# Performance work log

Hardware: AMD Instinct MI355X
Metric: run time of the kernel (lower is better)

Reference implementation:

```python
import jax, jax.numpy as jnp
import numpy as np

B, H, S, D = 8, 8, 2048, 64

def setup_inputs() -> dict:
    key = jax.random.key(0)
    kq, kk, kv = jax.random.split(key, 3)
    queries = jax.random.normal(kq, (B, H, S, D), dtype=jnp.float32)
    keys = jax.random.normal(kk, (B, H, S, D), dtype=jnp.float32)
    values = jax.random.normal(kv, (B, H, S, D), dtype=jnp.float32)
    return {"queries": queries, "keys": keys, "values": values}

def reference(queries, keys, values):
    # scores: [B,H,S,S] = Q K^T / sqrt(D)
    scale = 1.0 / jnp.sqrt(jnp.asarray(queries.shape[-1], dtype=jnp.float32))
    scores = jnp.einsum('bhqd,bhkd->bhqk', queries, keys) * scale
    attn = jax.nn.softmax(scores, axis=-1)
    # dropout is identity at eval (p=0.0)
    return jnp.einsum('bhqk,bhkd->bhqd', attn, values)
```

## Files before the change

kernel.cpp:

```cpp
#include <hip/hip_runtime.h>

#define S_LEN 2048
#define HEAD_D 64
#define NH 64
#define KVB 64
#define NKT (S_LEN / KVB)
#define RS 72
#define KREG (KVB * RS)
#define IMG_USH (2 * KREG)
#define IMG_B (IMG_USH * 2)
#define WS_V5 ((size_t)NH * NKT * IMG_B)
#define IMG4_USH (KVB * HEAD_D * 2)

typedef float f32x4  __attribute__((ext_vector_type(4)));
typedef float f32x16 __attribute__((ext_vector_type(16)));
typedef __bf16 bf16x8 __attribute__((ext_vector_type(8)));

static __device__ __forceinline__ unsigned short f2bf(float x) {
  __bf16 h = (__bf16)x;
  return __builtin_bit_cast(unsigned short, h);
}
static __device__ __forceinline__ void gload_lds16(const void* g, void* l) {
  __builtin_amdgcn_global_load_lds(
      (const __attribute__((address_space(1))) unsigned int*)g,
      (__attribute__((address_space(3))) unsigned int*)l, 16, 0, 0);
}
static __device__ __forceinline__ int vpos(int kv) {
  return (kv & ~15) | (((kv >> 2) & 1) << 3) | (((kv >> 3) & 1) << 2) | (kv & 3);
}

__global__ __launch_bounds__(256) void pack_kv5(
    const float* __restrict__ K, const float* __restrict__ V,
    unsigned short* __restrict__ ws)
{
  const int kt = blockIdx.x;
  const int bh = blockIdx.y;
  const int t  = threadIdx.x;
  const float* Kg = K + ((size_t)bh * S_LEN + (size_t)kt * KVB) * HEAD_D;
  const float* Vg = V + ((size_t)bh * S_LEN + (size_t)kt * KVB) * HEAD_D;
  unsigned short* img = ws + ((size_t)bh * NKT + kt) * IMG_USH;

  __shared__ unsigned short vt[KREG];

#pragma unroll
  for (int i = 0; i < 4; ++i) {
    const int e   = t * 4 + i * 1024;
    const int row = e >> 6;
    const int col = e & 63;
    float4 k4 = *(const float4*)(Kg + e);
    ushort4 kb;
    kb.x = f2bf(k4.x); kb.y = f2bf(k4.y); kb.z = f2bf(k4.z); kb.w = f2bf(k4.w);
    *(ushort4*)&img[row * RS + col] = kb;
    float4 v4 = *(const float4*)(Vg + e);
    const int p = vpos(row);
    vt[(col + 0) * RS + p] = f2bf(v4.x);
    vt[(col + 1) * RS + p] = f2bf(v4.y);
    vt[(col + 2) * RS + p] = f2bf(v4.z);
    vt[(col + 3) * RS + p] = f2bf(v4.w);
  }
  __syncthreads();
  char* dst = (char*)(img + KREG);
  const char* src = (const char*)vt;
#pragma unroll
  for (int i = 0; i < 3; ++i) {
    const int off = t * 16 + i * 4096;
    if (off < 9216) *(uint4*)(dst + off) = *(const uint4*)(src + off);
  }
}

#define QBLK 256
__global__ __launch_bounds__(256, 2) void flash_attn_fwd_v7(
    const float* __restrict__ Q, const unsigned short* __restrict__ ws,
    float* __restrict__ O)
{
  __shared__ unsigned short lds[4][IMG_USH];

  const int tid  = threadIdx.x;
  const int wave = tid >> 6;
  const int lane = tid & 63;
  const int l31  = lane & 31;
  const int hi   = lane >> 5;

  const int bid = blockIdx.x;
  const int swz = (bid & 7) * 64 + (bid >> 3);
  const int bh  = swz >> 3;
  const int qt  = swz & 7;

  const float* Qh = Q + (size_t)bh * (S_LEN * HEAD_D);
  float*       Oh = O + (size_t)bh * (S_LEN * HEAD_D);
  const char*  gbase = (const char*)(ws + (size_t)bh * NKT * IMG_USH);

  const int qrowA = qt * QBLK + wave * 64 + l31;
  const int qrowB = qrowA + 32;

  const float K2 = 0.18033688f;
  bf16x8 qfA[4], qfB[4];
#pragma unroll
  for (int c = 0; c < 4; ++c) {
    const float* qa = Qh + (size_t)qrowA * HEAD_D + c * 16 + hi * 8;
    float4 a0 = *(const float4*)qa;
    float4 a1 = *(const float4*)(qa + 4);
    qfA[c][0] = (__bf16)(a0.x * K2); qfA[c][1] = (__bf16)(a0.y * K2);
    qfA[c][2] = (__bf16)(a0.z * K2); qfA[c][3] = (__bf16)(a0.w * K2);
    qfA[c][4] = (__bf16)(a1.x * K2); qfA[c][5] = (__bf16)(a1.y * K2);
    qfA[c][6] = (__bf16)(a1.z * K2); qfA[c][7] = (__bf16)(a1.w * K2);
    const float* qb = Qh + (size_t)qrowB * HEAD_D + c * 16 + hi * 8;
    float4 b0 = *(const float4*)qb;
    float4 b1 = *(const float4*)(qb + 4);
    qfB[c][0] = (__bf16)(b0.x * K2); qfB[c][1] = (__bf16)(b0.y * K2);
    qfB[c][2] = (__bf16)(b0.z * K2); qfB[c][3] = (__bf16)(b0.w * K2);
    qfB[c][4] = (__bf16)(b1.x * K2); qfB[c][5] = (__bf16)(b1.y * K2);
    qfB[c][6] = (__bf16)(b1.z * K2); qfB[c][7] = (__bf16)(b1.w * K2);
  }

  bf16x8 onef;
#pragma unroll
  for (int i = 0; i < 8; ++i) onef[i] = (__bf16)1.0f;

  f32x16 oaA0, oaA1, oaB0, oaB1, oaLA, oaLB;
#pragma unroll
  for (int i = 0; i < 16; ++i) {
    oaA0[i] = 0.0f; oaA1[i] = 0.0f; oaB0[i] = 0.0f; oaB1[i] = 0.0f;
    oaLA[i] = 0.0f; oaLB[i] = 0.0f;
  }

  auto stage = [&](const char* g, unsigned short* Lp) {
    char* lb = (char*)Lp;
#pragma unroll
    for (int i = 0; i < 5; ++i) {
      const int ch = wave + i * 4;
      if (ch < 18) gload_lds16(g + ch * 1024 + lane * 16, lb + ch * 1024);
    }
  };

  auto compute = [&](const unsigned short* Lp) {
    const char* ka = (const char*)Lp + l31 * 144 + hi * 16;
    f32x16 p0A, p1A, p0B, p1B;
#pragma unroll
    for (int i = 0; i < 16; ++i) { p0A[i] = 0.0f; p1A[i] = 0.0f; p0B[i] = 0.0f; p1B[i] = 0.0f; }
    __builtin_amdgcn_s_setprio(1);
#pragma unroll
    for (int c = 0; c < 4; ++c) {
      bf16x8 kf0 = *(const bf16x8*)(ka + c * 32);
      bf16x8 kf1 = *(const bf16x8*)(ka + 4608 + c * 32);
      p0A = __builtin_amdgcn_mfma_f32_32x32x16_bf16(kf0, qfA[c], p0A, 0, 0, 0);
      p0B = __builtin_amdgcn_mfma_f32_32x32x16_bf16(kf0, qfB[c], p0B, 0, 0, 0);
      p1A = __builtin_amdgcn_mfma_f32_32x32x16_bf16(kf1, qfA[c], p1A, 0, 0, 0);
      p1B = __builtin_amdgcn_mfma_f32_32x32x16_bf16(kf1, qfB[c], p1B, 0, 0, 0);
    }
    __builtin_amdgcn_s_setprio(0);

#pragma unroll
    for (int i = 0; i < 16; ++i) {
      p0A[i] = __builtin_amdgcn_exp2f(p0A[i]);
      p1A[i] = __builtin_amdgcn_exp2f(p1A[i]);
      p0B[i] = __builtin_amdgcn_exp2f(p0B[i]);
      p1B[i] = __builtin_amdgcn_exp2f(p1B[i]);
    }

    __builtin_amdgcn_s_setprio(1);
#pragma unroll
    for (int kc = 0; kc < 4; ++kc) {
      const f32x16& psA = (kc < 2) ? p0A : p1A;
      const f32x16& psB = (kc < 2) ? p0B : p1B;
      const int rb = (kc & 1) * 8;
      unsigned a0, a1, a2, a3, b0, b1, b2, b3;
      asm("v_cvt_pk_bf16_f32 %0, %1, %2" : "=v"(a0) : "v"(psA[rb + 0]), "v"(psA[rb + 1]));
      asm("v_cvt_pk_bf16_f32 %0, %1, %2" : "=v"(a1) : "v"(psA[rb + 2]), "v"(psA[rb + 3]));
      asm("v_cvt_pk_bf16_f32 %0, %1, %2" : "=v"(a2) : "v"(psA[rb + 4]), "v"(psA[rb + 5]));
      asm("v_cvt_pk_bf16_f32 %0, %1, %2" : "=v"(a3) : "v"(psA[rb + 6]), "v"(psA[rb + 7]));
      asm("v_cvt_pk_bf16_f32 %0, %1, %2" : "=v"(b0) : "v"(psB[rb + 0]), "v"(psB[rb + 1]));
      asm("v_cvt_pk_bf16_f32 %0, %1, %2" : "=v"(b1) : "v"(psB[rb + 2]), "v"(psB[rb + 3]));
      asm("v_cvt_pk_bf16_f32 %0, %1, %2" : "=v"(b2) : "v"(psB[rb + 4]), "v"(psB[rb + 5]));
      asm("v_cvt_pk_bf16_f32 %0, %1, %2" : "=v"(b3) : "v"(psB[rb + 6]), "v"(psB[rb + 7]));
      uint4 wa; wa.x = a0; wa.y = a1; wa.z = a2; wa.w = a3;
      uint4 wb; wb.x = b0; wb.y = b1; wb.z = b2; wb.w = b3;
      bf16x8 pfA = __builtin_bit_cast(bf16x8, wa);
      bf16x8 pfB = __builtin_bit_cast(bf16x8, wb);
      bf16x8 vf0 = *(const bf16x8*)(ka + 9216 + kc * 32);
      bf16x8 vf1 = *(const bf16x8*)(ka + 9216 + 4608 + kc * 32);
      oaA0 = __builtin_amdgcn_mfma_f32_32x32x16_bf16(vf0, pfA, oaA0, 0, 0, 0);
      oaB0 = __builtin_amdgcn_mfma_f32_32x32x16_bf16(vf0, pfB, oaB0, 0, 0, 0);
      oaA1 = __builtin_amdgcn_mfma_f32_32x32x16_bf16(vf1, pfA, oaA1, 0, 0, 0);
      oaB1 = __builtin_amdgcn_mfma_f32_32x32x16_bf16(vf1, pfB, oaB1, 0, 0, 0);
      oaLA = __builtin_amdgcn_mfma_f32_32x32x16_bf16(onef, pfA, oaLA, 0, 0, 0);
      oaLB = __builtin_amdgcn_mfma_f32_32x32x16_bf16(onef, pfB, oaLB, 0, 0, 0);
    }
    __builtin_amdgcn_s_setprio(0);
  };

  stage(gbase, &lds[0][0]);
  stage(gbase + IMG_B, &lds[1][0]);
  __syncthreads();

  for (int kt = 0; kt < NKT; kt += 2) {
    const int cb = (kt & 2) ? 2 : 0;
    const int sb = cb ^ 2;
    const char* g2 = (kt + 2 < NKT) ? gbase + (size_t)(kt + 2) * IMG_B : gbase;
    const char* g3 = (kt + 3 < NKT) ? gbase + (size_t)(kt + 3) * IMG_B : gbase;
    stage(g2, &lds[sb][0]);
    stage(g3, &lds[sb + 1][0]);
    compute(&lds[cb][0]);
    compute(&lds[cb + 1][0]);
    __syncthreads();
  }

  const float invA = 1.0f / oaLA[0];
  const float invB = 1.0f / oaLB[0];
  float* orA = Oh + (size_t)qrowA * HEAD_D;
  float* orB = Oh + (size_t)qrowB * HEAD_D;
#pragma unroll
  for (int gg = 0; gg < 4; ++gg) {
    float4 o;
    o.x = oaA0[4 * gg + 0] * invA; o.y = oaA0[4 * gg + 1] * invA;
    o.z = oaA0[4 * gg + 2] * invA; o.w = oaA0[4 * gg + 3] * invA;
    *(float4*)&orA[gg * 8 + hi * 4] = o;
    o.x = oaA1[4 * gg + 0] * invA; o.y = oaA1[4 * gg + 1] * invA;
    o.z = oaA1[4 * gg + 2] * invA; o.w = oaA1[4 * gg + 3] * invA;
    *(float4*)&orA[32 + gg * 8 + hi * 4] = o;
    o.x = oaB0[4 * gg + 0] * invB; o.y = oaB0[4 * gg + 1] * invB;
    o.z = oaB0[4 * gg + 2] * invB; o.w = oaB0[4 * gg + 3] * invB;
    *(float4*)&orB[gg * 8 + hi * 4] = o;
    o.x = oaB1[4 * gg + 0] * invB; o.y = oaB1[4 * gg + 1] * invB;
    o.z = oaB1[4 * gg + 2] * invB; o.w = oaB1[4 * gg + 3] * invB;
    *(float4*)&orB[32 + gg * 8 + hi * 4] = o;
  }
}

__global__ __launch_bounds__(256) void pack_kv4(
    const float* __restrict__ K, const float* __restrict__ V,
    unsigned short* __restrict__ ws)
{
  const int kt = blockIdx.x;
  const int bh = blockIdx.y;
  const int t  = threadIdx.x;
  const float* Kg = K + ((size_t)bh * S_LEN + (size_t)kt * KVB) * HEAD_D;
  const float* Vg = V + ((size_t)bh * S_LEN + (size_t)kt * KVB) * HEAD_D;
  unsigned short* img = ws + ((size_t)bh * NKT + kt) * IMG4_USH;
  __shared__ unsigned short vt[HEAD_D * KVB];
#pragma unroll
  for (int i = 0; i < 4; ++i) {
    const int e   = t * 4 + i * 1024;
    const int row = e >> 6;
    const int col = e & 63;
    float4 k4 = *(const float4*)(Kg + e);
    ushort4 kb;
    kb.x = f2bf(k4.x); kb.y = f2bf(k4.y); kb.z = f2bf(k4.z); kb.w = f2bf(k4.w);
    *(ushort4*)&img[row * 64 + (col ^ ((row & 7) << 3))] = kb;
    float4 v4 = *(const float4*)(Vg + e);
    const int p = vpos(row);
    vt[(col + 0) * 64 + (p ^ (((col + 0) & 7) << 3))] = f2bf(v4.x);
    vt[(col + 1) * 64 + (p ^ (((col + 1) & 7) << 3))] = f2bf(v4.y);
    vt[(col + 2) * 64 + (p ^ (((col + 2) & 7) << 3))] = f2bf(v4.z);
    vt[(col + 3) * 64 + (p ^ (((col + 3) & 7) << 3))] = f2bf(v4.w);
  }
  __syncthreads();
  uint4* dst = (uint4*)(img + KVB * HEAD_D);
  const uint4* src = (const uint4*)vt;
#pragma unroll
  for (int i = 0; i < 2; ++i) dst[t + i * 256] = src[t + i * 256];
}

__global__ __launch_bounds__(256, 2) void flash_attn_fwd_v4(
    const float* __restrict__ Q, const unsigned short* __restrict__ ws,
    float* __restrict__ O)
{
  __shared__ unsigned short lds[2][IMG4_USH];
  const int tid  = threadIdx.x;
  const int wave = tid >> 6;
  const int lane = tid & 63;
  const int l31  = lane & 31;
  const int hi   = lane >> 5;
  const int bid = blockIdx.x;
  const int swz = (bid & 7) * 128 + (bid >> 3);
  const int bh  = swz >> 4;
  const int qt  = swz & 15;
  const float* Qh = Q + (size_t)bh * (S_LEN * HEAD_D);
  float*       Oh = O + (size_t)bh * (S_LEN * HEAD_D);
  const unsigned short* imgh = ws + (size_t)bh * NKT * IMG4_USH;
  const int qrow = qt * 128 + wave * 32 + l31;
  bf16x8 qf[4];
#pragma unroll
  for (int c = 0; c < 4; ++c) {
    const float* qp = Qh + (size_t)qrow * HEAD_D + c * 16 + hi * 8;
    float4 a = *(const float4*)qp;
    float4 b = *(const float4*)(qp + 4);
    qf[c][0] = (__bf16)a.x; qf[c][1] = (__bf16)a.y;
    qf[c][2] = (__bf16)a.z; qf[c][3] = (__bf16)a.w;
    qf[c][4] = (__bf16)b.x; qf[c][5] = (__bf16)b.y;
    qf[c][6] = (__bf16)b.z; qf[c][7] = (__bf16)b.w;
  }
  f32x16 oa0, oa1;
#pragma unroll
  for (int i = 0; i < 16; ++i) { oa0[i] = 0.0f; oa1[i] = 0.0f; }
  float m_run = -1e30f, l_run = 0.0f;
  const float SC = 0.125f;
  {
    const char* gg = (const char*)imgh;
    char* l = (char*)&lds[0][0];
    const int wb = wave * 4096;
#pragma unroll
    for (int c2 = 0; c2 < 4; ++c2) {
      const int off = wb + c2 * 1024;
      gload_lds16(gg + off + lane * 16, l + off);
    }
  }
  __syncthreads();
  int cur = 0;
  for (int kt = 0; kt < NKT; ++kt) {
    if (kt + 1 < NKT) {
      const char* gg = (const char*)(imgh + (size_t)(kt + 1) * IMG4_USH);
      char* l = (char*)&lds[cur ^ 1][0];
      const int wb = wave * 4096;
#pragma unroll
      for (int c2 = 0; c2 < 4; ++c2) {
        const int off = wb + c2 * 1024;
        gload_lds16(gg + off + lane * 16, l + off);
      }
    }
    const unsigned short* kT = &lds[cur][0];
    const unsigned short* vT = &lds[cur][KVB * HEAD_D];
    f32x16 p0, p1;
#pragma unroll
    for (int i = 0; i < 16; ++i) { p0[i] = 0.0f; p1[i] = 0.0f; }
    __builtin_amdgcn_s_setprio(1);
#pragma unroll
    for (int c = 0; c < 4; ++c) {
      const int r0 = l31;
      bf16x8 kf0 = *(const bf16x8*)&kT[r0 * 64 + ((c * 16 + hi * 8) ^ ((r0 & 7) << 3))];
      p0 = __builtin_amdgcn_mfma_f32_32x32x16_bf16(kf0, qf[c], p0, 0, 0, 0);
      const int r1 = l31 + 32;
      bf16x8 kf1 = *(const bf16x8*)&kT[r1 * 64 + ((c * 16 + hi * 8) ^ ((r1 & 7) << 3))];
      p1 = __builtin_amdgcn_mfma_f32_32x32x16_bf16(kf1, qf[c], p1, 0, 0, 0);
    }
    __builtin_amdgcn_s_setprio(0);
    float t16[16];
#pragma unroll
    for (int i = 0; i < 16; ++i) t16[i] = fmaxf(p0[i], p1[i]);
#pragma unroll
    for (int st = 8; st >= 1; st >>= 1)
#pragma unroll
      for (int i = 0; i < st; ++i) t16[i] = fmaxf(t16[i], t16[i + st]);
    const float tmax = fmaxf(t16[0], __shfl_xor(t16[0], 32));
    const int defer = __all((tmax - m_run) <= 64.0f);
    if (!defer) {
      const float mnew = fmaxf(m_run, tmax);
      const float corr = __expf((m_run - mnew) * SC);
      m_run = mnew;
      l_run *= corr;
#pragma unroll
      for (int i = 0; i < 16; ++i) { oa0[i] *= corr; oa1[i] *= corr; }
    }
    const float msc = m_run * SC;
#pragma unroll
    for (int i = 0; i < 16; ++i) {
      p0[i] = __expf(__builtin_fmaf(p0[i], SC, -msc));
      p1[i] = __expf(__builtin_fmaf(p1[i], SC, -msc));
    }
    float s16[16];
#pragma unroll
    for (int i = 0; i < 16; ++i) s16[i] = p0[i] + p1[i];
#pragma unroll
    for (int st = 8; st >= 1; st >>= 1)
#pragma unroll
      for (int i = 0; i < st; ++i) s16[i] = s16[i] + s16[i + st];
    l_run += s16[0] + __shfl_xor(s16[0], 32);
    __builtin_amdgcn_s_setprio(1);
#pragma unroll
    for (int kc = 0; kc < 4; ++kc) {
      const f32x16& ps = (kc < 2) ? p0 : p1;
      const int rb = (kc & 1) * 8;
      uint4 wv;
      wv.x = (unsigned)f2bf(ps[rb + 0]) | ((unsigned)f2bf(ps[rb + 1]) << 16);
      wv.y = (unsigned)f2bf(ps[rb + 2]) | ((unsigned)f2bf(ps[rb + 3]) << 16);
      wv.z = (unsigned)f2bf(ps[rb + 4]) | ((unsigned)f2bf(ps[rb + 5]) << 16);
      wv.w = (unsigned)f2bf(ps[rb + 6]) | ((unsigned)f2bf(ps[rb + 7]) << 16);
      bf16x8 pf = __builtin_bit_cast(bf16x8, wv);
#pragma unroll
      for (int db = 0; db < 2; ++db) {
        const int d = db * 32 + l31;
        bf16x8 vf = *(const bf16x8*)&vT[d * 64 + ((kc * 16 + hi * 8) ^ ((d & 7) << 3))];
        if (db == 0) oa0 = __builtin_amdgcn_mfma_f32_32x32x16_bf16(vf, pf, oa0, 0, 0, 0);
        else         oa1 = __builtin_amdgcn_mfma_f32_32x32x16_bf16(vf, pf, oa1, 0, 0, 0);
      }
    }
    __builtin_amdgcn_s_setprio(0);
    __syncthreads();
    cur ^= 1;
  }
  const float inv = 1.0f / l_run;
  float* orow = Oh + (size_t)qrow * HEAD_D;
#pragma unroll
  for (int gg = 0; gg < 4; ++gg) {
    float4 o4;
    o4.x = oa0[4 * gg + 0] * inv; o4.y = oa0[4 * gg + 1] * inv;
    o4.z = oa0[4 * gg + 2] * inv; o4.w = oa0[4 * gg + 3] * inv;
    *(float4*)&orow[gg * 8 + hi * 4] = o4;
    float4 o5;
    o5.x = oa1[4 * gg + 0] * inv; o5.y = oa1[4 * gg + 1] * inv;
    o5.z = oa1[4 * gg + 2] * inv; o5.w = oa1[4 * gg + 3] * inv;
    *(float4*)&orow[32 + gg * 8 + hi * 4] = o5;
  }
}

extern "C" void kernel_launch(void* const* d_in, const int* in_sizes, int n_in,
                              void* d_out, int out_size, void* d_ws, size_t ws_size,
                              hipStream_t stream) {
  const float* Q = (const float*)d_in[0];
  const float* K = (const float*)d_in[1];
  const float* V = (const float*)d_in[2];
  float* O = (float*)d_out;
  unsigned short* ws = (unsigned short*)d_ws;
  if (ws_size >= WS_V5) {
    hipLaunchKernelGGL(pack_kv5, dim3(NKT, NH), dim3(256), 0, stream, K, V, ws);
    hipLaunchKernelGGL(flash_attn_fwd_v7, dim3(512), dim3(256), 0, stream, Q, ws, O);
  } else {
    hipLaunchKernelGGL(pack_kv4, dim3(NKT, NH), dim3(256), 0, stream, K, V, ws);
    hipLaunchKernelGGL(flash_attn_fwd_v4, dim3(1024), dim3(256), 0, stream, Q, ws, O);
  }
}
```

Baseline: 101.4 us.

## Replace ones-MFMA row sums with VALU reduction and batch two QK^T tiles

New measurement: 105.5 us. +4.1%, slower.

```diff
diff --git a/kernel.cpp b/kernel.cpp
--- a/kernel.cpp
+++ b/kernel.cpp
@@ -69,7 +69,7 @@
 }
 
 #define QBLK 256
-__global__ __launch_bounds__(256, 2) void flash_attn_fwd_v7(
+__global__ __launch_bounds__(256, 2) void flash_attn_fwd_v8(
     const float* __restrict__ Q, const unsigned short* __restrict__ ws,
     float* __restrict__ O)
 {
@@ -113,16 +113,10 @@
     qfB[c][6] = (__bf16)(b1.z * K2); qfB[c][7] = (__bf16)(b1.w * K2);
   }
 
-  bf16x8 onef;
-#pragma unroll
-  for (int i = 0; i < 8; ++i) onef[i] = (__bf16)1.0f;
-
-  f32x16 oaA0, oaA1, oaB0, oaB1, oaLA, oaLB;
-#pragma unroll
-  for (int i = 0; i < 16; ++i) {
-    oaA0[i] = 0.0f; oaA1[i] = 0.0f; oaB0[i] = 0.0f; oaB1[i] = 0.0f;
-    oaLA[i] = 0.0f; oaLB[i] = 0.0f;
-  }
+  f32x16 oaA0, oaA1, oaB0, oaB1;
+#pragma unroll
+  for (int i = 0; i < 16; ++i) { oaA0[i] = 0.0f; oaA1[i] = 0.0f; oaB0[i] = 0.0f; oaB1[i] = 0.0f; }
+  float lA = 0.0f, lB = 0.0f;
 
   auto stage = [&](const char* g, unsigned short* Lp) {
     char* lb = (char*)Lp;
@@ -133,9 +127,9 @@
     }
   };
 
-  auto compute = [&](const unsigned short* Lp) {
+  auto qkt = [&](const unsigned short* Lp,
+                 f32x16& p0A, f32x16& p1A, f32x16& p0B, f32x16& p1B) {
     const char* ka = (const char*)Lp + l31 * 144 + hi * 16;
-    f32x16 p0A, p1A, p0B, p1B;
 #pragma unroll
     for (int i = 0; i < 16; ++i) { p0A[i] = 0.0f; p1A[i] = 0.0f; p0B[i] = 0.0f; p1B[i] = 0.0f; }
     __builtin_amdgcn_s_setprio(1);
@@ -149,7 +143,11 @@
       p1B = __builtin_amdgcn_mfma_f32_32x32x16_bf16(kf1, qfB[c], p1B, 0, 0, 0);
     }
     __builtin_amdgcn_s_setprio(0);
-
+  };
+
+  auto finish = [&](const unsigned short* Lp,
+                    f32x16& p0A, f32x16& p1A, f32x16& p0B, f32x16& p1B) {
+    const char* ka = (const char*)Lp + l31 * 144 + hi * 16;
 #pragma unroll
     for (int i = 0; i < 16; ++i) {
       p0A[i] = __builtin_amdgcn_exp2f(p0A[i]);
@@ -157,6 +155,15 @@
       p0B[i] = __builtin_amdgcn_exp2f(p0B[i]);
       p1B[i] = __builtin_amdgcn_exp2f(p1B[i]);
     }
+    float sA[16], sB[16];
+#pragma unroll
+    for (int i = 0; i < 16; ++i) { sA[i] = p0A[i] + p1A[i]; sB[i] = p0B[i] + p1B[i]; }
+#pragma unroll
+    for (int st = 8; st >= 1; st >>= 1)
+#pragma unroll
+      for (int i = 0; i < st; ++i) { sA[i] += sA[i + st]; sB[i] += sB[i + st]; }
+    lA += sA[0];
+    lB += sB[0];
 
     __builtin_amdgcn_s_setprio(1);
 #pragma unroll
@@ -183,8 +190,6 @@
       oaB0 = __builtin_amdgcn_mfma_f32_32x32x16_bf16(vf0, pfB, oaB0, 0, 0, 0);
       oaA1 = __builtin_amdgcn_mfma_f32_32x32x16_bf16(vf1, pfA, oaA1, 0, 0, 0);
       oaB1 = __builtin_amdgcn_mfma_f32_32x32x16_bf16(vf1, pfB, oaB1, 0, 0, 0);
-      oaLA = __builtin_amdgcn_mfma_f32_32x32x16_bf16(onef, pfA, oaLA, 0, 0, 0);
-      oaLB = __builtin_amdgcn_mfma_f32_32x32x16_bf16(onef, pfB, oaLB, 0, 0, 0);
     }
     __builtin_amdgcn_s_setprio(0);
   };
@@ -200,13 +205,18 @@
     const char* g3 = (kt + 3 < NKT) ? gbase + (size_t)(kt + 3) * IMG_B : gbase;
     stage(g2, &lds[sb][0]);
     stage(g3, &lds[sb + 1][0]);
-    compute(&lds[cb][0]);
-    compute(&lds[cb + 1][0]);
+
+    f32x16 x0A, x1A, x0B, x1B;
+    f32x16 y0A, y1A, y0B, y1B;
+    qkt(&lds[cb][0],     x0A, x1A, x0B, x1B);
+    qkt(&lds[cb + 1][0], y0A, y1A, y0B, y1B);
+    finish(&lds[cb][0],     x0A, x1A, x0B, x1B);
+    finish(&lds[cb + 1][0], y0A, y1A, y0B, y1B);
     __syncthreads();
   }
 
-  const float invA = 1.0f / oaLA[0];
-  const float invB = 1.0f / oaLB[0];
+  const float invA = 1.0f / (lA + __shfl_xor(lA, 32));
+  const float invB = 1.0f / (lB + __shfl_xor(lB, 32));
   float* orA = Oh + (size_t)qrowA * HEAD_D;
   float* orB = Oh + (size_t)qrowB * HEAD_D;
 #pragma unroll
@@ -413,7 +423,7 @@
   unsigned short* ws = (unsigned short*)d_ws;
   if (ws_size >= WS_V5) {
     hipLaunchKernelGGL(pack_kv5, dim3(NKT, NH), dim3(256), 0, stream, K, V, ws);
-    hipLaunchKernelGGL(flash_attn_fwd_v7, dim3(512), dim3(256), 0, stream, Q, ws, O);
+    hipLaunchKernelGGL(flash_attn_fwd_v8, dim3(512), dim3(256), 0, stream, Q, ws, O);
   } else {
     hipLaunchKernelGGL(pack_kv4, dim3(NKT, NH), dim3(256), 0, stream, K, V, ws);
     hipLaunchKernelGGL(flash_attn_fwd_v4, dim3(1024), dim3(256), 0, stream, Q, ws, O);
```
